# Kernel optimization log

Measured on AMD Instinct MI355X. Metric: run time of the kernel, lower is better.

## Reference

```python
import jax, jax.numpy as jnp
from jax import lax
import numpy as np

T, D, DFF, E, K = 1024, 2048, 1024, 16, 6


def setup_inputs() -> dict:
    key = jax.random.key(0)
    ks = jax.random.split(key, 9)
    x = jax.random.normal(ks[0], (T, D), dtype=jnp.float32)
    selected_experts = jax.random.randint(ks[1], (T, K), 0, E, dtype=jnp.int64)
    rw = jax.random.uniform(ks[2], (T, K), dtype=jnp.float32)
    routing_weights = rw / jnp.sum(rw, axis=-1, keepdims=True)  # normalized top-k weights
    # Expert weights: w0 (gate), w1 (up): [E, DFF, D]; w2 (down): [E, D, DFF]
    w0 = jax.random.normal(ks[3], (E, DFF, D), dtype=jnp.float32) * (D ** -0.5)
    w1 = jax.random.normal(ks[4], (E, DFF, D), dtype=jnp.float32) * (D ** -0.5)
    w2 = jax.random.normal(ks[5], (E, D, DFF), dtype=jnp.float32) * (DFF ** -0.5)
    # Per-expert dequant scales (s0/s1/s2 in the fused kernel)
    s0 = jax.random.uniform(ks[6], (E,), dtype=jnp.float32, minval=0.5, maxval=1.5)
    s1 = jax.random.uniform(ks[7], (E,), dtype=jnp.float32, minval=0.5, maxval=1.5)
    s2 = jax.random.uniform(ks[8], (E,), dtype=jnp.float32, minval=0.5, maxval=1.5)
    return {"x": x, "w0": w0, "w1": w1, "w2": w2, "s0": s0, "s1": s1, "s2": s2,
            "selected_experts": selected_experts, "routing_weights": routing_weights}


def reference(x, w0, w1, w2, s0, s1, s2, selected_experts, routing_weights):
    num_experts = w0.shape[0]
    # combine weights per (token, expert): sum of routing weights over top-k slots
    onehot = jax.nn.one_hot(selected_experts, num_experts, dtype=x.dtype)  # [T,K,E]
    cw = jnp.einsum('tke,tk->et', onehot, routing_weights)                 # [E,T]

    def body(acc, inp):
        w0e, w1e, w2e, s0e, s1e, s2e, cwe = inp
        g = (x @ w0e.T) * s0e                 # [T,DFF] gate proj (dequant scale)
        u = (x @ w1e.T) * s1e                 # [T,DFF] up proj
        h = jax.nn.silu(g) * u                # SwiGLU
        y = (h @ w2e.T) * s2e                 # [T,D] down proj
        return acc + cwe[:, None] * y, None

    out, _ = lax.scan(body, jnp.zeros_like(x), (w0, w1, w2, s0, s1, s2, cw))
    return out
```

## Files before the change

### kernel.cpp

```cpp
#include <hip/hip_runtime.h>
#include <hip/hip_bf16.h>
#include <stdint.h>

#define T_TOK 1024
#define D_DIM 2048
#define DFF   1024
#define NE    16
#define TOPK  6

typedef float f32x4 __attribute__((ext_vector_type(4)));
typedef __bf16 bf16x8 __attribute__((ext_vector_type(8)));
typedef unsigned short u16x8 __attribute__((ext_vector_type(8)));

__device__ __forceinline__ unsigned short f2bf(float f) {
    union { float f; unsigned int u; } v; v.f = f;
    unsigned int x = v.u;
    unsigned int r = x + 0x7FFFu + ((x >> 16) & 1u);
    return (unsigned short)(r >> 16);
}

__device__ __forceinline__ unsigned int pack_bf2(float x, float y) {
    unsigned int a = __builtin_bit_cast(unsigned int, x) + 0x8000u;
    unsigned int b = __builtin_bit_cast(unsigned int, y) + 0x8000u;
    return __builtin_amdgcn_perm(b, a, 0x07060302);
}
__device__ __forceinline__ u16x8 cvt8(float4 p, float4 q) {
    union { u16x8 v; unsigned int w[4]; } u;
    u.w[0] = pack_bf2(p.x, p.y);
    u.w[1] = pack_bf2(p.z, p.w);
    u.w[2] = pack_bf2(q.x, q.y);
    u.w[3] = pack_bf2(q.z, q.w);
    return u.v;
}


__global__ void cw_scatter(const int* __restrict__ sel,
                           const float* __restrict__ rw,
                           float* __restrict__ cw) {
    int i = blockIdx.x * blockDim.x + threadIdx.x;
    if (i < T_TOK * TOPK) {
        int t = i / TOPK;
        int e = sel[i];
        atomicAdd(&cw[e * T_TOK + t], rw[i]);
    }
}

__global__ void build_lists(const float* __restrict__ cw,
                            int* __restrict__ list,
                            int* __restrict__ count) {
    int i = blockIdx.x * blockDim.x + threadIdx.x;
    if (i < NE * T_TOK) {
        int e = i >> 10;
        float c = cw[i];
        if (c != 0.f) {
            int p = atomicAdd(&count[e], 1);
            list[(e << 10) + p] = i & 1023;
        }
    }
}

__global__ __launch_bounds__(256, 2)
void gemm1_kernel(const float* __restrict__ xf,
                  const float* __restrict__ w0,
                  const float* __restrict__ w1,
                  const float* __restrict__ cw,
                  const int* __restrict__ list,
                  const int* __restrict__ count,
                  const float* __restrict__ s0,
                  const float* __restrict__ s1,
                  const float* __restrict__ s2,
                  unsigned short* __restrict__ hc)
{
    const int tf = blockIdx.x, tile = blockIdx.y, e = blockIdx.z;
    const int n_e = count[e];
    const int base = tile * 128;
    if (base >= n_e) return;

    const int tid = threadIdx.x;
    const int lane = tid & 63, wid = tid >> 6;
    const int wm = wid >> 1, wn = wid & 1;
    const int quad = lane >> 4, l16 = lane & 15;

    __shared__ alignas(16) unsigned short sA [128 * 64];
    __shared__ alignas(16) unsigned short sB0[128 * 64];
    __shared__ alignas(16) unsigned short sB1[128 * 64];
    __shared__ int   slist[128];
    __shared__ float cws[128];

    if (tid < 128) {
        int idx = base + tid;
        int cl = idx < n_e ? idx : (n_e - 1);
        int tok = list[(e << 10) + cl];
        slist[tid] = tok;
        cws[tid] = (idx < n_e) ? cw[e * T_TOK + tok] : 0.f;
    }
    __syncthreads();

    int rowtok[4];
#pragma unroll
    for (int it = 0; it < 4; ++it) rowtok[it] = slist[it * 32 + (tid >> 3)];

    const float* b0_base = w0 + ((size_t)e * DFF + tf * 128) * D_DIM;
    const float* b1_base = w1 + ((size_t)e * DFF + tf * 128) * D_DIM;

    f32x4 accG[4][4], accU[4][4];
    const f32x4 zz = {0.f, 0.f, 0.f, 0.f};
#pragma unroll
    for (int mi = 0; mi < 4; ++mi)
#pragma unroll
        for (int ni = 0; ni < 4; ++ni) { accG[mi][ni] = zz; accU[mi][ni] = zz; }

    for (int k0 = 0; k0 < D_DIM; k0 += 64) {
        u16x8 rA[4], rB0[4], rB1[4];
#pragma unroll
        for (int it = 0; it < 4; ++it) {
            int c = it * 256 + tid;
            int row = c >> 3, col = c & 7;
            const float* ap = xf + (size_t)rowtok[it] * D_DIM + k0 + col * 8;
            float4 a0 = *(const float4*)ap, a1 = *(const float4*)(ap + 4);
            const float* bp0 = b0_base + (size_t)row * D_DIM + k0 + col * 8;
            float4 b00 = *(const float4*)bp0, b01 = *(const float4*)(bp0 + 4);
            const float* bp1 = b1_base + (size_t)row * D_DIM + k0 + col * 8;
            float4 b10 = *(const float4*)bp1, b11 = *(const float4*)(bp1 + 4);
            rA [it] = cvt8(a0, a1);
            rB0[it] = cvt8(b00, b01);
            rB1[it] = cvt8(b10, b11);
        }
        __syncthreads();
#pragma unroll
        for (int it = 0; it < 4; ++it) {
            int c = it * 256 + tid;
            int row = c >> 3, col = c & 7;
            int cs = col ^ (row & 7);
            *(u16x8*)(sA  + row * 64 + cs * 8) = rA [it];
            *(u16x8*)(sB0 + row * 64 + cs * 8) = rB0[it];
            *(u16x8*)(sB1 + row * 64 + cs * 8) = rB1[it];
        }
        __syncthreads();
#pragma unroll
        for (int kk = 0; kk < 2; ++kk) {
            bf16x8 af[4], b0f[4], b1f[4];
#pragma unroll
            for (int mi = 0; mi < 4; ++mi) {
                int row = wm * 64 + mi * 16 + l16;
                int cch = (kk * 4 + quad) ^ (row & 7);
                af[mi] = __builtin_bit_cast(bf16x8,
                         *(const u16x8*)(sA + row * 64 + cch * 8));
            }
#pragma unroll
            for (int ni = 0; ni < 4; ++ni) {
                int row = wn * 64 + ni * 16 + l16;
                int cch = (kk * 4 + quad) ^ (row & 7);
                b0f[ni] = __builtin_bit_cast(bf16x8,
                          *(const u16x8*)(sB0 + row * 64 + cch * 8));
                b1f[ni] = __builtin_bit_cast(bf16x8,
                          *(const u16x8*)(sB1 + row * 64 + cch * 8));
            }
#pragma unroll
            for (int mi = 0; mi < 4; ++mi)
#pragma unroll
                for (int ni = 0; ni < 4; ++ni) {
                    accG[mi][ni] = __builtin_amdgcn_mfma_f32_16x16x32_bf16(
                        af[mi], b0f[ni], accG[mi][ni], 0, 0, 0);
                    accU[mi][ni] = __builtin_amdgcn_mfma_f32_16x16x32_bf16(
                        af[mi], b1f[ni], accU[mi][ni], 0, 0, 0);
                }
        }
    }

    const float s0e = s0[e], s1e = s1[e], s2e = s2[e];
#pragma unroll
    for (int mi = 0; mi < 4; ++mi) {
#pragma unroll
        for (int reg = 0; reg < 4; ++reg) {
            int tl = wm * 64 + mi * 16 + quad * 4 + reg;
            float cwt = cws[tl] * s2e;
            size_t slot = (size_t)((e << 10) + base + tl);
#pragma unroll
            for (int ni = 0; ni < 4; ++ni) {
                float g = accG[mi][ni][reg] * s0e;
                float u = accU[mi][ni][reg] * s1e;
                float h = g / (1.f + __expf(-g)) * u;
                int fc = tf * 128 + wn * 64 + ni * 16 + l16;
                hc[slot * DFF + fc] = f2bf(h * cwt);
            }
        }
    }
}

__global__ __launch_bounds__(256, 2)
void gemm2_kernel(const unsigned short* __restrict__ hc,
                  const float* __restrict__ w2,
                  const int* __restrict__ list,
                  const int* __restrict__ count,
                  float* __restrict__ out)
{
    const int td = blockIdx.x, tile = blockIdx.y, e = blockIdx.z;
    const int n_e = count[e];
    const int base = tile * 128;
    if (base >= n_e) return;

    const int tid = threadIdx.x;
    const int lane = tid & 63, wid = tid >> 6;
    const int wm = wid >> 1, wn = wid & 1;
    const int quad = lane >> 4, l16 = lane & 15;

    __shared__ alignas(16) unsigned short sA[128 * 64];
    __shared__ alignas(16) unsigned short sB[128 * 64];
    __shared__ int slist[128];

    if (tid < 128) {
        int idx = base + tid;
        int cl = idx < n_e ? idx : (n_e - 1);
        slist[tid] = list[(e << 10) + cl];
    }
    __syncthreads();

    const unsigned short* a_base = hc + (size_t)((e << 10) + base) * DFF;
    const float* b_base = w2 + ((size_t)e * D_DIM + td * 128) * DFF;

    f32x4 acc[4][4];
    const f32x4 zz = {0.f, 0.f, 0.f, 0.f};
#pragma unroll
    for (int mi = 0; mi < 4; ++mi)
#pragma unroll
        for (int ni = 0; ni < 4; ++ni) acc[mi][ni] = zz;

    for (int k0 = 0; k0 < DFF; k0 += 64) {
        u16x8 rA[4], rB[4];
#pragma unroll
        for (int it = 0; it < 4; ++it) {
            int c = it * 256 + tid;
            int row = c >> 3, col = c & 7;
            rA[it] = *(const u16x8*)(a_base + (size_t)row * DFF + k0 + col * 8);
            const float* bp = b_base + (size_t)row * DFF + k0 + col * 8;
            float4 b0 = *(const float4*)bp, b1 = *(const float4*)(bp + 4);
            rB[it] = cvt8(b0, b1);
        }
        __syncthreads();
#pragma unroll
        for (int it = 0; it < 4; ++it) {
            int c = it * 256 + tid;
            int row = c >> 3, col = c & 7;
            int cs = col ^ (row & 7);
            *(u16x8*)(sA + row * 64 + cs * 8) = rA[it];
            *(u16x8*)(sB + row * 64 + cs * 8) = rB[it];
        }
        __syncthreads();
#pragma unroll
        for (int kk = 0; kk < 2; ++kk) {
            bf16x8 af[4], bfr[4];
#pragma unroll
            for (int mi = 0; mi < 4; ++mi) {
                int row = wm * 64 + mi * 16 + l16;
                int cch = (kk * 4 + quad) ^ (row & 7);
                af[mi] = __builtin_bit_cast(bf16x8,
                         *(const u16x8*)(sA + row * 64 + cch * 8));
            }
#pragma unroll
            for (int ni = 0; ni < 4; ++ni) {
                int row = wn * 64 + ni * 16 + l16;
                int cch = (kk * 4 + quad) ^ (row & 7);
                bfr[ni] = __builtin_bit_cast(bf16x8,
                          *(const u16x8*)(sB + row * 64 + cch * 8));
            }
#pragma unroll
            for (int mi = 0; mi < 4; ++mi)
#pragma unroll
                for (int ni = 0; ni < 4; ++ni)
                    acc[mi][ni] = __builtin_amdgcn_mfma_f32_16x16x32_bf16(
                        af[mi], bfr[ni], acc[mi][ni], 0, 0, 0);
        }
    }

#pragma unroll
    for (int mi = 0; mi < 4; ++mi)
#pragma unroll
        for (int reg = 0; reg < 4; ++reg) {
            int tl = wm * 64 + mi * 16 + quad * 4 + reg;
            if (base + tl < n_e) {
                int tok = slist[tl];
                float* orow = out + (size_t)tok * D_DIM;
#pragma unroll
                for (int ni = 0; ni < 4; ++ni) {
                    int d = td * 128 + wn * 64 + ni * 16 + l16;
                    atomicAdd(orow + d, acc[mi][ni][reg]);
                }
            }
        }
}


extern "C" void kernel_launch(void* const* d_in, const int* in_sizes, int n_in,
                              void* d_out, int out_size, void* d_ws, size_t ws_size,
                              hipStream_t stream) {
    const float* x  = (const float*)d_in[0];
    const float* w0 = (const float*)d_in[1];
    const float* w1 = (const float*)d_in[2];
    const float* w2 = (const float*)d_in[3];
    const float* s0 = (const float*)d_in[4];
    const float* s1 = (const float*)d_in[5];
    const float* s2 = (const float*)d_in[6];
    const int*   sel = (const int*)d_in[7];
    const float* rw = (const float*)d_in[8];
    float* out = (float*)d_out;

    char* ws = (char*)d_ws;
    constexpr size_t HC_OFF    = 0;
    constexpr size_t LIST_OFF  = 33554432ull;
    constexpr size_t CW_OFF    = LIST_OFF + 65536ull;
    constexpr size_t COUNT_OFF = CW_OFF + 65536ull;
    unsigned short* hc    = (unsigned short*)(ws + HC_OFF);
    int*            list  = (int*)           (ws + LIST_OFF);
    float*          cw    = (float*)         (ws + CW_OFF);
    int*            count = (int*)           (ws + COUNT_OFF);

    hipMemsetAsync(cw, 0, 65536 + 256, stream);
    cw_scatter<<<(T_TOK * TOPK + 255) / 256, 256, 0, stream>>>(sel, rw, cw);
    build_lists<<<(NE * T_TOK + 255) / 256, 256, 0, stream>>>(cw, list, count);

    hipMemsetAsync(out, 0, (size_t)T_TOK * D_DIM * sizeof(float), stream);

    gemm1_kernel<<<dim3(DFF / 128, T_TOK / 128, NE), 256, 0, stream>>>(
        x, w0, w1, cw, list, count, s0, s1, s2, hc);

    gemm2_kernel<<<dim3(D_DIM / 128, T_TOK / 128, NE), 256, 0, stream>>>(
        hc, w2, list, count, out);
}
```

Before: 558.6 us.

## Pre-convert weights and activations to bf16 and merge routing into one kernel

After: 534.8 us. -4.3%, faster.

```diff
diff --git a/kernel.cpp b/kernel.cpp
--- a/kernel.cpp
+++ b/kernel.cpp
@@ -19,50 +19,54 @@
     return (unsigned short)(r >> 16);
 }
 
-__device__ __forceinline__ unsigned int pack_bf2(float x, float y) {
-    unsigned int a = __builtin_bit_cast(unsigned int, x) + 0x8000u;
-    unsigned int b = __builtin_bit_cast(unsigned int, y) + 0x8000u;
-    return __builtin_amdgcn_perm(b, a, 0x07060302);
-}
-__device__ __forceinline__ u16x8 cvt8(float4 p, float4 q) {
-    union { u16x8 v; unsigned int w[4]; } u;
-    u.w[0] = pack_bf2(p.x, p.y);
-    u.w[1] = pack_bf2(p.z, p.w);
-    u.w[2] = pack_bf2(q.x, q.y);
-    u.w[3] = pack_bf2(q.z, q.w);
-    return u.v;
-}
-
-
-__global__ void cw_scatter(const int* __restrict__ sel,
-                           const float* __restrict__ rw,
-                           float* __restrict__ cw) {
+__global__ void cvt_f32_bf16(const float* __restrict__ src,
+                             unsigned short* __restrict__ dst, int n4) {
     int i = blockIdx.x * blockDim.x + threadIdx.x;
-    if (i < T_TOK * TOPK) {
-        int t = i / TOPK;
-        int e = sel[i];
-        atomicAdd(&cw[e * T_TOK + t], rw[i]);
-    }
-}
-
-__global__ void build_lists(const float* __restrict__ cw,
-                            int* __restrict__ list,
-                            int* __restrict__ count) {
-    int i = blockIdx.x * blockDim.x + threadIdx.x;
-    if (i < NE * T_TOK) {
-        int e = i >> 10;
-        float c = cw[i];
+    int stride = gridDim.x * blockDim.x;
+    for (; i < n4; i += stride) {
+        float4 v = ((const float4*)src)[i];
+        ushort4 o;
+        o.x = f2bf(v.x); o.y = f2bf(v.y); o.z = f2bf(v.z); o.w = f2bf(v.w);
+        ((ushort4*)dst)[i] = o;
+    }
+}
+
+__global__ __launch_bounds__(1024)
+void routing_kernel(const int* __restrict__ sel,
+                    const float* __restrict__ rw,
+                    float* __restrict__ cw,
+                    int* __restrict__ list,
+                    int* __restrict__ count) {
+    __shared__ float scw[NE * T_TOK];
+    __shared__ int scount[NE];
+    const int t = threadIdx.x;
+#pragma unroll
+    for (int e = 0; e < NE; ++e) scw[e * T_TOK + t] = 0.f;
+    if (t < NE) scount[t] = 0;
+    __syncthreads();
+#pragma unroll
+    for (int k = 0; k < TOPK; ++k) {
+        int e = sel[t * TOPK + k];
+        scw[e * T_TOK + t] += rw[t * TOPK + k];
+    }
+    __syncthreads();
+#pragma unroll
+    for (int e = 0; e < NE; ++e) {
+        float c = scw[e * T_TOK + t];
+        cw[e * T_TOK + t] = c;
         if (c != 0.f) {
-            int p = atomicAdd(&count[e], 1);
-            list[(e << 10) + p] = i & 1023;
-        }
-    }
+            int p = atomicAdd(&scount[e], 1);
+            list[(e << 10) + p] = t;
+        }
+    }
+    __syncthreads();
+    if (t < NE) count[t] = scount[t];
 }
 
 __global__ __launch_bounds__(256, 2)
-void gemm1_kernel(const float* __restrict__ xf,
-                  const float* __restrict__ w0,
-                  const float* __restrict__ w1,
+void gemm1_kernel(const unsigned short* __restrict__ xb,
+                  const unsigned short* __restrict__ wb0,
+                  const unsigned short* __restrict__ wb1,
                   const float* __restrict__ cw,
                   const int* __restrict__ list,
                   const int* __restrict__ count,
@@ -100,8 +104,8 @@
 #pragma unroll
     for (int it = 0; it < 4; ++it) rowtok[it] = slist[it * 32 + (tid >> 3)];
 
-    const float* b0_base = w0 + ((size_t)e * DFF + tf * 128) * D_DIM;
-    const float* b1_base = w1 + ((size_t)e * DFF + tf * 128) * D_DIM;
+    const unsigned short* b0_base = wb0 + ((size_t)e * DFF + tf * 128) * D_DIM;
+    const unsigned short* b1_base = wb1 + ((size_t)e * DFF + tf * 128) * D_DIM;
 
     f32x4 accG[4][4], accU[4][4];
     const f32x4 zz = {0.f, 0.f, 0.f, 0.f};
@@ -116,15 +120,9 @@
         for (int it = 0; it < 4; ++it) {
             int c = it * 256 + tid;
             int row = c >> 3, col = c & 7;
-            const float* ap = xf + (size_t)rowtok[it] * D_DIM + k0 + col * 8;
-            float4 a0 = *(const float4*)ap, a1 = *(const float4*)(ap + 4);
-            const float* bp0 = b0_base + (size_t)row * D_DIM + k0 + col * 8;
-            float4 b00 = *(const float4*)bp0, b01 = *(const float4*)(bp0 + 4);
-            const float* bp1 = b1_base + (size_t)row * D_DIM + k0 + col * 8;
-            float4 b10 = *(const float4*)bp1, b11 = *(const float4*)(bp1 + 4);
-            rA [it] = cvt8(a0, a1);
-            rB0[it] = cvt8(b00, b01);
-            rB1[it] = cvt8(b10, b11);
+            rA [it] = *(const u16x8*)(xb + (size_t)rowtok[it] * D_DIM + k0 + col * 8);
+            rB0[it] = *(const u16x8*)(b0_base + (size_t)row * D_DIM + k0 + col * 8);
+            rB1[it] = *(const u16x8*)(b1_base + (size_t)row * D_DIM + k0 + col * 8);
         }
         __syncthreads();
 #pragma unroll
@@ -190,7 +188,7 @@
 
 __global__ __launch_bounds__(256, 2)
 void gemm2_kernel(const unsigned short* __restrict__ hc,
-                  const float* __restrict__ w2,
+                  const unsigned short* __restrict__ wb2,
                   const int* __restrict__ list,
                   const int* __restrict__ count,
                   float* __restrict__ out)
@@ -217,7 +215,7 @@
     __syncthreads();
 
     const unsigned short* a_base = hc + (size_t)((e << 10) + base) * DFF;
-    const float* b_base = w2 + ((size_t)e * D_DIM + td * 128) * DFF;
+    const unsigned short* b_base = wb2 + ((size_t)e * D_DIM + td * 128) * DFF;
 
     f32x4 acc[4][4];
     const f32x4 zz = {0.f, 0.f, 0.f, 0.f};
@@ -233,9 +231,7 @@
             int c = it * 256 + tid;
             int row = c >> 3, col = c & 7;
             rA[it] = *(const u16x8*)(a_base + (size_t)row * DFF + k0 + col * 8);
-            const float* bp = b_base + (size_t)row * DFF + k0 + col * 8;
-            float4 b0 = *(const float4*)bp, b1 = *(const float4*)(bp + 4);
-            rB[it] = cvt8(b0, b1);
+            rB[it] = *(const u16x8*)(b_base + (size_t)row * DFF + k0 + col * 8);
         }
         __syncthreads();
 #pragma unroll
@@ -306,24 +302,35 @@
     float* out = (float*)d_out;
 
     char* ws = (char*)d_ws;
-    constexpr size_t HC_OFF    = 0;
-    constexpr size_t LIST_OFF  = 33554432ull;
+    constexpr size_t W0B_OFF   = 0;
+    constexpr size_t W1B_OFF   = 67108864ull;
+    constexpr size_t XB_OFF    = 134217728ull;
+    constexpr size_t HC_OFF    = 138412032ull;
+    constexpr size_t LIST_OFF  = 171966464ull;
     constexpr size_t CW_OFF    = LIST_OFF + 65536ull;
     constexpr size_t COUNT_OFF = CW_OFF + 65536ull;
+    unsigned short* w0b   = (unsigned short*)(ws + W0B_OFF);
+    unsigned short* w1b   = (unsigned short*)(ws + W1B_OFF);
+    unsigned short* w2b   = (unsigned short*)(ws + W0B_OFF);
+    unsigned short* xb    = (unsigned short*)(ws + XB_OFF);
     unsigned short* hc    = (unsigned short*)(ws + HC_OFF);
     int*            list  = (int*)           (ws + LIST_OFF);
     float*          cw    = (float*)         (ws + CW_OFF);
     int*            count = (int*)           (ws + COUNT_OFF);
 
-    hipMemsetAsync(cw, 0, 65536 + 256, stream);
-    cw_scatter<<<(T_TOK * TOPK + 255) / 256, 256, 0, stream>>>(sel, rw, cw);
-    build_lists<<<(NE * T_TOK + 255) / 256, 256, 0, stream>>>(cw, list, count);
+    routing_kernel<<<1, 1024, 0, stream>>>(sel, rw, cw, list, count);
 
     hipMemsetAsync(out, 0, (size_t)T_TOK * D_DIM * sizeof(float), stream);
 
+    cvt_f32_bf16<<<4096, 256, 0, stream>>>(w0, w0b, NE * DFF * D_DIM / 4);
+    cvt_f32_bf16<<<4096, 256, 0, stream>>>(w1, w1b, NE * DFF * D_DIM / 4);
+    cvt_f32_bf16<<<1024, 256, 0, stream>>>(x,  xb,  T_TOK * D_DIM / 4);
+
     gemm1_kernel<<<dim3(DFF / 128, T_TOK / 128, NE), 256, 0, stream>>>(
-        x, w0, w1, cw, list, count, s0, s1, s2, hc);
+        xb, w0b, w1b, cw, list, count, s0, s1, s2, hc);
+
+    cvt_f32_bf16<<<4096, 256, 0, stream>>>(w2, w2b, NE * D_DIM * DFF / 4);
 
     gemm2_kernel<<<dim3(D_DIM / 128, T_TOK / 128, NE), 256, 0, stream>>>(
-        hc, w2, list, count, out);
-}
+        hc, w2b, list, count, out);
+}
```
